# Kernel tuning notes

Measured on AMD Instinct MI355X. Metric: run time of the kernel, lower is better.

Reference implementation:

```python
import jax, jax.numpy as jnp
import numpy as np

N, E, D, H, B = 10000, 160000, 128, 1, 4
SLOPE = 0.01  # negative_slope from DeepQNet default


def gat_layer(x, node_state, src, dst, W, att_src, att_dst, Wns, bns, bias):
    # x: [N,D] or [B,N,D]; node_state: [B,N,1]
    xs = x + node_state @ Wns + bns              # [B,N,D]
    Bx, Nn = xs.shape[0], xs.shape[1]
    h = (xs @ W).reshape(Bx, Nn, H, D)           # [B,N,H,C]
    a_src = (h * att_src).sum(-1)                # [B,N,H]
    a_dst = (h * att_dst).sum(-1)                # [B,N,H]
    ae = a_src[:, src] + a_dst[:, dst]           # [B,Etot,H]
    ae = jnp.where(ae > 0, ae, SLOPE * ae)       # leaky_relu
    ae_t = jnp.moveaxis(ae, 1, 0)                # [Etot,B,H]
    m = jax.ops.segment_max(ae_t, dst, num_segments=Nn)   # [N,B,H]
    e = jnp.exp(ae_t - m[dst])
    s = jax.ops.segment_sum(e, dst, num_segments=Nn)
    alpha = e / s[dst]                           # [Etot,B,H]
    h_e = jnp.moveaxis(h, 1, 0)                  # [N,B,H,C]
    msg = alpha[..., None] * h_e[src]            # [Etot,B,H,C]
    out = jax.ops.segment_sum(msg, dst, num_segments=Nn)  # [N,B,H,C]
    out = jnp.moveaxis(out, 0, 1).mean(2) + bias # concat=False -> head mean
    return jax.nn.relu(out)


def setup_inputs() -> dict:
    key = jax.random.key(0)
    ks = jax.random.split(key, 16)
    edges = jax.random.randint(ks[0], (2, E), 0, N)
    loop = jnp.arange(N)
    edge_index = jnp.concatenate([edges, jnp.stack([loop, loop])], axis=1)  # add_self_loops
    state = jax.random.uniform(ks[1], (B, N), dtype=jnp.float32)
    strucEmb = jax.random.normal(ks[2], (N, D), dtype=jnp.float32) * 0.1
    s = 0.05
    return {
        "state": state,
        "strucEmb": strucEmb,
        "edge_index": edge_index,
        "gat_W": jax.random.normal(ks[3], (3, D, H * D), dtype=jnp.float32) * s,
        "gat_att_src": jax.random.normal(ks[4], (3, H, D), dtype=jnp.float32) * s,
        "gat_att_dst": jax.random.normal(ks[5], (3, H, D), dtype=jnp.float32) * s,
        "gat_Wns": jax.random.normal(ks[6], (3, 1, D), dtype=jnp.float32) * s,
        "gat_bns": jnp.zeros((3, D), jnp.float32),
        "gat_bias": jnp.zeros((3, D), jnp.float32),
        "W1": jax.random.normal(ks[7], (D, D), dtype=jnp.float32) * s,
        "b1": jnp.zeros((D,), jnp.float32),
        "W2": jax.random.normal(ks[8], (D, D), dtype=jnp.float32) * s,
        "b2": jnp.zeros((D,), jnp.float32),
        "W3": jax.random.normal(ks[9], (2 * D, 1), dtype=jnp.float32) * s,
        "b3": jnp.zeros((1,), jnp.float32),
    }


def reference(state, strucEmb, edge_index, gat_W, gat_att_src, gat_att_dst,
              gat_Wns, gat_bns, gat_bias, W1, b1, W2, b2, W3, b3):
    src, dst = edge_index[0], edge_index[1]
    rs = state.reshape(state.shape[0], N, 1)     # [B,N,1]
    x = strucEmb
    for l in range(3):
        x = gat_layer(x, rs, src, dst, gat_W[l], gat_att_src[l], gat_att_dst[l],
                      gat_Wns[l], gat_bns[l], gat_bias[l])
    state_emb = x.sum(1)                         # [B,D]
    beta_state = state_emb @ W1 + b1             # [B,D]
    beta_action = x @ W2 + b2                    # [B,N,D]  (is_for_learn=True path)
    expand_state = jnp.broadcast_to(beta_state[:, None, :], beta_action.shape)
    out = jax.nn.relu(jnp.concatenate([expand_state, beta_action], axis=2))
    return out @ W3 + b3                         # [B,N,1]
```

## Files before the change

kernel.cpp:

```cpp
#include <hip/hip_runtime.h>
#include <math.h>

#define N_NODES 10000
#define B_SZ 4
#define SLOPE 0.01f
#define BN (B_SZ * N_NODES)
#define PADK 136

typedef __attribute__((ext_vector_type(8))) short short8;
typedef __attribute__((ext_vector_type(4))) float float4v;

__device__ __forceinline__ unsigned short f2bf(float f) {
    unsigned u = __builtin_bit_cast(unsigned, f);
    u += 0x7fffu + ((u >> 16) & 1u);
    return (unsigned short)(u >> 16);
}
__device__ __forceinline__ float bf2f(unsigned short s) {
    unsigned u = ((unsigned)s) << 16;
    return __builtin_bit_cast(float, u);
}
__device__ __forceinline__ float bflo(unsigned u) { return __builtin_bit_cast(float, u << 16); }
__device__ __forceinline__ float bfhi(unsigned u) { return __builtin_bit_cast(float, u & 0xffff0000u); }



__global__ __launch_bounds__(256) void setup_kernel(
    const float* __restrict__ strucEmb, const float* __restrict__ state,
    const float* __restrict__ Wns0, const float* __restrict__ bns0,
    const float* __restrict__ gatW, const float* __restrict__ W2,
    unsigned short* __restrict__ XS,
    unsigned short* __restrict__ whi, unsigned short* __restrict__ wlo,
    int* deg, int* cursor, float* state_emb)
{
    int bx = blockIdx.x, tid = threadIdx.x;
    if (bx < 2500) {
        int base = (bx * 256 + tid) * 8;
        int g = base >> 7, d0 = base & 127;
        int n = g - (g / N_NODES) * N_NODES;
        float st = state[g];
        const float* se = strucEmb + (size_t)n * 128 + d0;
        const float* wp = Wns0 + d0;
        const float* bp = bns0 + d0;
        short8 v;
#pragma unroll
        for (int j = 0; j < 8; j++)
            v[j] = (short)f2bf(se[j] + st * wp[j] + bp[j]);
        *(short8*)(XS + base) = v;
    } else if (bx < 2756) {
        int i = (bx - 2500) * 256 + tid;
        int w = i >> 14, rem = i & 16383;
        int k = rem >> 7, c = rem & 127;
        const float* src = (w < 3) ? (gatW + (size_t)w * 16384) : W2;
        float v = src[k * 128 + c];
        unsigned short h = f2bf(v);
        whi[w * 16384 + c * 128 + k] = h;
        wlo[w * 16384 + c * 128 + k] = f2bf(v - bf2f(h));
    } else {
        int i = (bx - 2756) * 256 + tid;
        if (i < N_NODES) { deg[i] = 0; cursor[i] = 0; }
        if (i < 512) state_emb[i] = 0.f;
    }
}


__global__ __launch_bounds__(256) void hist_kernel(const int* __restrict__ dst, int Etot, int* deg) {
    int e = blockIdx.x * 256 + threadIdx.x;
    if (e < Etot) atomicAdd(&deg[dst[e]], 1);
}

__global__ __launch_bounds__(1024) void scan_kernel(const int* __restrict__ deg, int* __restrict__ rowOff) {
    __shared__ int wsum[16];
    int tid = threadIdx.x;
    int lane = tid & 63, wid = tid >> 6;
    int base = tid * 10;
    int v[10]; int tot = 0;
#pragma unroll
    for (int j = 0; j < 10; j++) {
        int idx = base + j;
        int d = (idx < N_NODES) ? deg[idx] : 0;
        tot += d; v[j] = tot;
    }
    int incl = tot;
    for (int off = 1; off < 64; off <<= 1) {
        int t = __shfl_up(incl, off, 64);
        if (lane >= off) incl += t;
    }
    if (lane == 63) wsum[wid] = incl;
    __syncthreads();
    if (wid == 0) {
        int wv = (lane < 16) ? wsum[lane] : 0;
        for (int off = 1; off < 16; off <<= 1) {
            int t = __shfl_up(wv, off, 64);
            if (lane >= off) wv += t;
        }
        if (lane < 16) wsum[lane] = wv;
    }
    __syncthreads();
    int waveoff = (wid > 0) ? wsum[wid - 1] : 0;
    int excl = waveoff + incl - tot;
    if (tid == 0) rowOff[0] = 0;
#pragma unroll
    for (int j = 0; j < 10; j++) {
        int idx = base + j;
        if (idx < N_NODES) rowOff[idx + 1] = excl + v[j];
    }
}

__global__ __launch_bounds__(256) void scatter_kernel(const int* __restrict__ src, const int* __restrict__ dst,
                                                      int Etot, const int* __restrict__ rowOff,
                                                      int* cursor, int* __restrict__ srcLst) {
    int e = blockIdx.x * 256 + threadIdx.x;
    if (e < Etot) {
        int d = dst[e];
        int pos = rowOff[d] + atomicAdd(&cursor[d], 1);
        srcLst[pos] = src[e];
    }
}


__global__ __launch_bounds__(256) void gemm_att_mfma(
    const unsigned short* __restrict__ XS,
    const unsigned short* __restrict__ WThi, const unsigned short* __restrict__ WTlo,
    const float* __restrict__ attS, const float* __restrict__ attD,
    unsigned short* __restrict__ Hout, float* __restrict__ aSrcP, float* __restrict__ aDstP)
{
    __shared__ __align__(16) unsigned short sCus[64 * PADK];
    __shared__ float sAs[128], sAd[128];
    __shared__ float sPart[64 * 8];

    int tid = threadIdx.x;
    int g0 = blockIdx.x * 64;
    int w = tid >> 6, lane = tid & 63;
    int quad = lane >> 4, mcol = lane & 15;

    if (tid < 128) { sAs[tid] = attS[tid]; sAd[tid] = attD[tid]; }

    float4v acc[4][2];
#pragma unroll
    for (int mt = 0; mt < 4; mt++)
#pragma unroll
        for (int nt = 0; nt < 2; nt++) acc[mt][nt] = (float4v){0.f, 0.f, 0.f, 0.f};

#pragma unroll 1
    for (int term = 0; term < 2; term++) {
        const unsigned short* WT = term ? WTlo : WThi;
        short8 Bf[4][2];
#pragma unroll
        for (int kc = 0; kc < 4; kc++)
#pragma unroll
            for (int nt = 0; nt < 2; nt++)
                Bf[kc][nt] = *(const short8*)(WT + (w * 32 + nt * 16 + mcol) * 128 + kc * 32 + quad * 8);
#pragma unroll
        for (int kc = 0; kc < 4; kc++) {
            short8 Aa[4];
#pragma unroll
            for (int mt = 0; mt < 4; mt++)
                Aa[mt] = *(const short8*)(XS + (size_t)(g0 + mt * 16 + mcol) * 128 + kc * 32 + quad * 8);
#pragma unroll
            for (int mt = 0; mt < 4; mt++)
#pragma unroll
                for (int nt = 0; nt < 2; nt++)
                    acc[mt][nt] = __builtin_amdgcn_mfma_f32_16x16x32_bf16(Aa[mt], Bf[kc][nt], acc[mt][nt], 0, 0, 0);
        }
    }

    __syncthreads();

    float pp[16], pd[16];
#pragma unroll
    for (int r16 = 0; r16 < 16; r16++) { pp[r16] = 0.f; pd[r16] = 0.f; }
#pragma unroll
    for (int mt = 0; mt < 4; mt++)
#pragma unroll
        for (int nt = 0; nt < 2; nt++)
#pragma unroll
            for (int reg = 0; reg < 4; reg++) {
                int row = mt * 16 + quad * 4 + reg;
                int col = w * 32 + nt * 16 + mcol;
                float v = acc[mt][nt][reg];
                sCus[row * PADK + col] = f2bf(v);
                pp[mt * 4 + reg] += v * sAs[col];
                pd[mt * 4 + reg] += v * sAd[col];
            }
#pragma unroll
    for (int off = 1; off < 16; off <<= 1)
#pragma unroll
        for (int r16 = 0; r16 < 16; r16++) {
            pp[r16] += __shfl_xor(pp[r16], off);
            pd[r16] += __shfl_xor(pd[r16], off);
        }
    if (mcol == 0) {
#pragma unroll
        for (int r16 = 0; r16 < 16; r16++) {
            int row = (r16 >> 2) * 16 + quad * 4 + (r16 & 3);
            sPart[row * 8 + w * 2 + 0] = pp[r16];
            sPart[row * 8 + w * 2 + 1] = pd[r16];
        }
    }
    __syncthreads();

    for (int i = tid; i < 64 * 16; i += 256) {
        int r = i >> 4, c8 = i & 15;
        uint4 u = *(uint4*)(sCus + r * PADK + c8 * 8);
        *(uint4*)(Hout + (size_t)(g0 + r) * 128 + c8 * 8) = u;
    }
    if (tid < 64) {
        float s0 = sPart[tid * 8] + sPart[tid * 8 + 2] + sPart[tid * 8 + 4] + sPart[tid * 8 + 6];
        float s1 = sPart[tid * 8 + 1] + sPart[tid * 8 + 3] + sPart[tid * 8 + 5] + sPart[tid * 8 + 7];
        aSrcP[g0 + tid] = s0;
        aDstP[g0 + tid] = s1;
    }
}


__global__ __launch_bounds__(256) void sm_agg_kernel(
    const int* __restrict__ rowOff, const int* __restrict__ srcLst,
    const float* __restrict__ aSrcP, const float* __restrict__ aDstP,
    const unsigned short* __restrict__ H,
    const float* __restrict__ bias,
    const float* __restrict__ state, const float* __restrict__ wnsN,
    const float* __restrict__ bnsN, int addNext,
    unsigned short* __restrict__ Xout)
{
    __shared__ int   sSrcB[4 * 64];
    __shared__ float sAeB[4 * 64];
    int tid = threadIdx.x;
    int w = tid >> 6, t = tid & 63;
    int blk = blockIdx.x;
    int xcd = blk & 7;
    int b = xcd >> 1;
    int n = (((xcd & 1) * (N_NODES / 8) + (blk >> 3)) << 2) + w;
    int gb = b * N_NODES;
    int start = rowOff[n], end = rowOff[n + 1];
    int cnt = end - start;
    float adst = aDstP[gb + n];
    int*   sSrc = sSrcB + w * 64;
    float* sAe  = sAeB + w * 64;
    const uint4* H4 = (const uint4*)H;

    if (cnt <= 64) {
        float ae = -1e30f;
        if (t < cnt) {
            int sn = srcLst[start + t];
            sSrc[t] = sn;
            float v = aSrcP[gb + sn] + adst;
            ae = v > 0.f ? v : SLOPE * v;
        }
        float m = ae;
        m = fmaxf(m, __shfl_xor(m, 1));  m = fmaxf(m, __shfl_xor(m, 2));
        m = fmaxf(m, __shfl_xor(m, 4));  m = fmaxf(m, __shfl_xor(m, 8));
        m = fmaxf(m, __shfl_xor(m, 16)); m = fmaxf(m, __shfl_xor(m, 32));
        float e = (t < cnt) ? __expf(ae - m) : 0.f;
        float s = e;
        s += __shfl_xor(s, 1);  s += __shfl_xor(s, 2);  s += __shfl_xor(s, 4);
        s += __shfl_xor(s, 8);  s += __shfl_xor(s, 16); s += __shfl_xor(s, 32);
        float inv = 1.f / s;
        if (t < cnt) sAe[t] = e * inv;
        int cntE = (cnt + 3) & ~3;
        if (t >= cnt && t < cntE) { sSrc[t] = n; sAe[t] = 0.f; }

        int esub = t >> 4, c16 = t & 15;
        float a0 = 0.f, a1 = 0.f, a2 = 0.f, a3 = 0.f, a4 = 0.f, a5 = 0.f, a6 = 0.f, a7 = 0.f;
        int j = 0;
        for (; j + 16 <= cntE; j += 16) {
            uint4 h[4]; float al[4];
#pragma unroll
            for (int r = 0; r < 4; r++) {
                int jj = j + r * 4 + esub;
                h[r] = H4[(size_t)(gb + sSrc[jj]) * 16 + c16];
                al[r] = sAe[jj];
            }
#pragma unroll
            for (int r = 0; r < 4; r++) {
                a0 += al[r] * bflo(h[r].x); a1 += al[r] * bfhi(h[r].x);
                a2 += al[r] * bflo(h[r].y); a3 += al[r] * bfhi(h[r].y);
                a4 += al[r] * bflo(h[r].z); a5 += al[r] * bfhi(h[r].z);
                a6 += al[r] * bflo(h[r].w); a7 += al[r] * bfhi(h[r].w);
            }
        }
        for (; j < cntE; j += 4) {
            int jj = j + esub;
            uint4 hv = H4[(size_t)(gb + sSrc[jj]) * 16 + c16];
            float al = sAe[jj];
            a0 += al * bflo(hv.x); a1 += al * bfhi(hv.x);
            a2 += al * bflo(hv.y); a3 += al * bfhi(hv.y);
            a4 += al * bflo(hv.z); a5 += al * bfhi(hv.z);
            a6 += al * bflo(hv.w); a7 += al * bfhi(hv.w);
        }
        a0 += __shfl_xor(a0, 16); a1 += __shfl_xor(a1, 16);
        a2 += __shfl_xor(a2, 16); a3 += __shfl_xor(a3, 16);
        a4 += __shfl_xor(a4, 16); a5 += __shfl_xor(a5, 16);
        a6 += __shfl_xor(a6, 16); a7 += __shfl_xor(a7, 16);
        a0 += __shfl_xor(a0, 32); a1 += __shfl_xor(a1, 32);
        a2 += __shfl_xor(a2, 32); a3 += __shfl_xor(a3, 32);
        a4 += __shfl_xor(a4, 32); a5 += __shfl_xor(a5, 32);
        a6 += __shfl_xor(a6, 32); a7 += __shfl_xor(a7, 32);
        if (esub == 0) {
            int d0 = c16 * 8;
            float o0 = fmaxf(a0 + bias[d0],     0.f);
            float o1 = fmaxf(a1 + bias[d0 + 1], 0.f);
            float o2 = fmaxf(a2 + bias[d0 + 2], 0.f);
            float o3 = fmaxf(a3 + bias[d0 + 3], 0.f);
            float o4 = fmaxf(a4 + bias[d0 + 4], 0.f);
            float o5 = fmaxf(a5 + bias[d0 + 5], 0.f);
            float o6 = fmaxf(a6 + bias[d0 + 6], 0.f);
            float o7 = fmaxf(a7 + bias[d0 + 7], 0.f);
            if (addNext) {
                float st = state[gb + n];
                o0 += st * wnsN[d0]     + bnsN[d0];
                o1 += st * wnsN[d0 + 1] + bnsN[d0 + 1];
                o2 += st * wnsN[d0 + 2] + bnsN[d0 + 2];
                o3 += st * wnsN[d0 + 3] + bnsN[d0 + 3];
                o4 += st * wnsN[d0 + 4] + bnsN[d0 + 4];
                o5 += st * wnsN[d0 + 5] + bnsN[d0 + 5];
                o6 += st * wnsN[d0 + 6] + bnsN[d0 + 6];
                o7 += st * wnsN[d0 + 7] + bnsN[d0 + 7];
            }
            uint4 u;
            u.x = (unsigned)f2bf(o0) | ((unsigned)f2bf(o1) << 16);
            u.y = (unsigned)f2bf(o2) | ((unsigned)f2bf(o3) << 16);
            u.z = (unsigned)f2bf(o4) | ((unsigned)f2bf(o5) << 16);
            u.w = (unsigned)f2bf(o6) | ((unsigned)f2bf(o7) << 16);
            ((uint4*)Xout)[(size_t)(gb + n) * 16 + c16] = u;
        }
    } else {
        const unsigned* Hu = (const unsigned*)H;
        float m = -1e30f;
        for (int i = start + t; i < end; i += 64) {
            int sn = srcLst[i];
            float v = aSrcP[gb + sn] + adst;
            m = fmaxf(m, v > 0.f ? v : SLOPE * v);
        }
        m = fmaxf(m, __shfl_xor(m, 1));  m = fmaxf(m, __shfl_xor(m, 2));
        m = fmaxf(m, __shfl_xor(m, 4));  m = fmaxf(m, __shfl_xor(m, 8));
        m = fmaxf(m, __shfl_xor(m, 16)); m = fmaxf(m, __shfl_xor(m, 32));
        float s = 0.f;
        for (int i = start + t; i < end; i += 64) {
            int sn = srcLst[i];
            float v = aSrcP[gb + sn] + adst;
            float ae2 = v > 0.f ? v : SLOPE * v;
            s += __expf(ae2 - m);
        }
        s += __shfl_xor(s, 1);  s += __shfl_xor(s, 2);  s += __shfl_xor(s, 4);
        s += __shfl_xor(s, 8);  s += __shfl_xor(s, 16); s += __shfl_xor(s, 32);
        float inv = 1.f / s;
        float accx = 0.f, accy = 0.f;
        for (int c0 = start; c0 < end; c0 += 64) {
            int c = min(64, end - c0);
            if (t < c) {
                int sn = srcLst[c0 + t];
                sSrc[t] = sn;
                float v = aSrcP[gb + sn] + adst;
                float ae2 = v > 0.f ? v : SLOPE * v;
                sAe[t] = __expf(ae2 - m);
            }
            for (int j = 0; j < c; j++) {
                float a0 = sAe[j];
                unsigned h0 = Hu[(size_t)(gb + sSrc[j]) * 64 + t];
                accx += a0 * bflo(h0);
                accy += a0 * bfhi(h0);
            }
        }
        float ox = fmaxf(accx * inv + bias[2 * t], 0.f);
        float oy = fmaxf(accy * inv + bias[2 * t + 1], 0.f);
        if (addNext) {
            float st = state[gb + n];
            ox += st * wnsN[2 * t]     + bnsN[2 * t];
            oy += st * wnsN[2 * t + 1] + bnsN[2 * t + 1];
        }
        ((unsigned*)Xout)[(size_t)(gb + n) * 64 + t] =
            (unsigned)f2bf(ox) | ((unsigned)f2bf(oy) << 16);
    }
}


__global__ __launch_bounds__(128) void sum_nodes_kernel(const unsigned short* __restrict__ X, float* state_emb) {
    int cx = blockIdx.x, b = blockIdx.y, d = threadIdx.x;
    int n0 = cx * 157, n1 = n0 + 157;
    if (n1 > N_NODES) n1 = N_NODES;
    float acc = 0.f;
    for (int n = n0; n < n1; n++) acc += bf2f(X[(size_t)(b * N_NODES + n) * 128 + d]);
    atomicAdd(&state_emb[b * 128 + d], acc);
}


__global__ __launch_bounds__(256) void final_mfma(
    const unsigned short* __restrict__ X,
    const unsigned short* __restrict__ WThi, const unsigned short* __restrict__ WTlo,
    const float* __restrict__ b2, const float* __restrict__ W3,
    const float* __restrict__ b3,
    const float* __restrict__ state_emb, const float* __restrict__ W1,
    const float* __restrict__ b1,
    float* __restrict__ out)
{
    __shared__ float sB2[128], sW3[128];
    __shared__ float sPart[64 * 4];
    __shared__ float sC1p[8], sC1[4];

    int tid = threadIdx.x;
    int g0 = blockIdx.x * 64;
    int w = tid >> 6, lane = tid & 63;
    int quad = lane >> 4, mcol = lane & 15;

    if (tid < 128) { sB2[tid] = b2[tid]; sW3[tid] = W3[128 + tid]; }

    {
        int d = tid & 127;
        int bh = tid >> 7;
        float p0 = b1[d], p1 = b1[d];
        for (int k = 0; k < 128; k++) {
            float wv = W1[k * 128 + d];
            p0 += state_emb[bh * 128 + k] * wv;
            p1 += state_emb[(bh + 2) * 128 + k] * wv;
        }
        float w3d = W3[d];
        p0 = fmaxf(p0, 0.f) * w3d;
        p1 = fmaxf(p1, 0.f) * w3d;
#pragma unroll
        for (int off = 1; off < 64; off <<= 1) {
            p0 += __shfl_xor(p0, off);
            p1 += __shfl_xor(p1, off);
        }
        if (lane == 0) { sC1p[w * 2 + 0] = p0; sC1p[w * 2 + 1] = p1; }
    }
    __syncthreads();
    if (tid == 0) {
        sC1[0] = sC1p[0] + sC1p[2];  sC1[2] = sC1p[1] + sC1p[3];
        sC1[1] = sC1p[4] + sC1p[6];  sC1[3] = sC1p[5] + sC1p[7];
    }

    float4v acc[4][2];
#pragma unroll
    for (int mt = 0; mt < 4; mt++)
#pragma unroll
        for (int nt = 0; nt < 2; nt++) acc[mt][nt] = (float4v){0.f, 0.f, 0.f, 0.f};

#pragma unroll 1
    for (int term = 0; term < 2; term++) {
        const unsigned short* WT = term ? WTlo : WThi;
        short8 Bf[4][2];
#pragma unroll
        for (int kc = 0; kc < 4; kc++)
#pragma unroll
            for (int nt = 0; nt < 2; nt++)
                Bf[kc][nt] = *(const short8*)(WT + (w * 32 + nt * 16 + mcol) * 128 + kc * 32 + quad * 8);
#pragma unroll
        for (int kc = 0; kc < 4; kc++) {
            short8 Aa[4];
#pragma unroll
            for (int mt = 0; mt < 4; mt++)
                Aa[mt] = *(const short8*)(X + (size_t)(g0 + mt * 16 + mcol) * 128 + kc * 32 + quad * 8);
#pragma unroll
            for (int mt = 0; mt < 4; mt++)
#pragma unroll
                for (int nt = 0; nt < 2; nt++)
                    acc[mt][nt] = __builtin_amdgcn_mfma_f32_16x16x32_bf16(Aa[mt], Bf[kc][nt], acc[mt][nt], 0, 0, 0);
        }
    }

    float pp[16];
#pragma unroll
    for (int r16 = 0; r16 < 16; r16++) pp[r16] = 0.f;
#pragma unroll
    for (int mt = 0; mt < 4; mt++)
#pragma unroll
        for (int nt = 0; nt < 2; nt++)
#pragma unroll
            for (int reg = 0; reg < 4; reg++) {
                int col = w * 32 + nt * 16 + mcol;
                float v = acc[mt][nt][reg] + sB2[col];
                v = v > 0.f ? v : 0.f;
                pp[mt * 4 + reg] += v * sW3[col];
            }
#pragma unroll
    for (int off = 1; off < 16; off <<= 1)
#pragma unroll
        for (int r16 = 0; r16 < 16; r16++)
            pp[r16] += __shfl_xor(pp[r16], off);
    if (mcol == 0) {
#pragma unroll
        for (int r16 = 0; r16 < 16; r16++) {
            int row = (r16 >> 2) * 16 + quad * 4 + (r16 & 3);
            sPart[row * 4 + w] = pp[r16];
        }
    }
    __syncthreads();
    if (tid < 64) {
        float p = sPart[tid * 4] + sPart[tid * 4 + 1] + sPart[tid * 4 + 2] + sPart[tid * 4 + 3];
        int g = g0 + tid;
        int b = g / N_NODES;
        out[g] = p + sC1[b] + b3[0];
    }
}


extern "C" void kernel_launch(void* const* d_in, const int* in_sizes, int n_in,
                              void* d_out, int out_size, void* d_ws, size_t ws_size,
                              hipStream_t stream) {
    const float* state    = (const float*)d_in[0];
    const float* strucEmb = (const float*)d_in[1];
    const int*   edge_idx = (const int*)d_in[2];
    const float* gat_W    = (const float*)d_in[3];
    const float* gat_aS   = (const float*)d_in[4];
    const float* gat_aD   = (const float*)d_in[5];
    const float* gat_Wns  = (const float*)d_in[6];
    const float* gat_bns  = (const float*)d_in[7];
    const float* gat_bias = (const float*)d_in[8];
    const float* W1 = (const float*)d_in[9];
    const float* b1 = (const float*)d_in[10];
    const float* W2 = (const float*)d_in[11];
    const float* b2 = (const float*)d_in[12];
    const float* W3 = (const float*)d_in[13];
    const float* b3 = (const float*)d_in[14];
    float* out = (float*)d_out;

    int Etot = in_sizes[2] / 2;
    const int* srcArr = edge_idx;
    const int* dstArr = edge_idx + Etot;

    float* ws = (float*)d_ws;
    unsigned short* Xb = (unsigned short*)ws;
    unsigned short* Hb = (unsigned short*)(ws + 2560000);
    float* aSrcP       = ws + 5120000;
    float* aDstP       = ws + 5160000;
    float* state_emb   = ws + 5200000;
    unsigned short* whi = (unsigned short*)(ws + 5200516);
    unsigned short* wlo = whi + 4 * 16384;
    int*   iws         = (int*)(ws + 5200516 + 65536);
    int*   rowOff      = iws;
    int*   deg         = iws + 10001;
    int*   cursor      = deg + 10000;
    int*   srcLst      = cursor + 10000;

    setup_kernel<<<2796, 256, 0, stream>>>(strucEmb, state, gat_Wns, gat_bns,
                                           gat_W, W2, Xb, whi, wlo, deg, cursor, state_emb);
    hist_kernel<<<(Etot + 255) / 256, 256, 0, stream>>>(dstArr, Etot, deg);
    scan_kernel<<<1, 1024, 0, stream>>>(deg, rowOff);
    scatter_kernel<<<(Etot + 255) / 256, 256, 0, stream>>>(srcArr, dstArr, Etot, rowOff, cursor, srcLst);

    for (int l = 0; l < 3; l++) {
        gemm_att_mfma<<<BN / 64, 256, 0, stream>>>(
            Xb, whi + (size_t)l * 16384, wlo + (size_t)l * 16384,
            gat_aS + l * 128, gat_aD + l * 128, Hb, aSrcP, aDstP);
        sm_agg_kernel<<<N_NODES, 256, 0, stream>>>(
            rowOff, srcLst, aSrcP, aDstP, Hb, gat_bias + l * 128,
            state, gat_Wns + (l + 1 < 3 ? (l + 1) * 128 : 0),
            gat_bns + (l + 1 < 3 ? (l + 1) * 128 : 0), (l < 2) ? 1 : 0, Xb);
    }

    sum_nodes_kernel<<<dim3(64, B_SZ), 128, 0, stream>>>(Xb, state_emb);
    final_mfma<<<BN / 64, 256, 0, stream>>>(Xb, whi + 3 * 16384, wlo + 3 * 16384,
                                            b2, W3, b3, state_emb, W1, b1, out);
}
```

Baseline: 323.4 us.

## Fuse per-layer GEMM, aggregation and final head into one persistent kernel

Replaces the eight per-layer and final kernel launches with one persistent kernel of 512 blocks. The blocks loop over GEMM tiles and aggregation items and separate phases with a software grid barrier built on global atomics. This removes launch overhead and the gaps between kernels. In exchange it relies on all 512 blocks being co-resident, which risks deadlock if they are not, and it limits parallelism per phase to the fixed grid.

```diff
diff --git a/kernel.cpp b/kernel.cpp
--- a/kernel.cpp
+++ b/kernel.cpp
@@ -6,6 +6,7 @@
 #define SLOPE 0.01f
 #define BN (B_SZ * N_NODES)
 #define PADK 136
+#define GRID_P 512
 
 typedef __attribute__((ext_vector_type(8))) short short8;
 typedef __attribute__((ext_vector_type(4))) float float4v;
@@ -21,6 +22,24 @@
 }
 __device__ __forceinline__ float bflo(unsigned u) { return __builtin_bit_cast(float, u << 16); }
 __device__ __forceinline__ float bfhi(unsigned u) { return __builtin_bit_cast(float, u & 0xffff0000u); }
+
+__device__ __forceinline__ void grid_barrier(int* counter, int* gen) {
+    __syncthreads();
+    if (threadIdx.x == 0) {
+        __threadfence();
+        int g0 = __hip_atomic_load(gen, __ATOMIC_RELAXED, __HIP_MEMORY_SCOPE_AGENT);
+        int arrived = __hip_atomic_fetch_add(counter, 1, __ATOMIC_ACQ_REL, __HIP_MEMORY_SCOPE_AGENT);
+        if (arrived == GRID_P - 1) {
+            __hip_atomic_store(counter, 0, __ATOMIC_RELAXED, __HIP_MEMORY_SCOPE_AGENT);
+            __hip_atomic_store(gen, g0 + 1, __ATOMIC_RELEASE, __HIP_MEMORY_SCOPE_AGENT);
+        } else {
+            while (__hip_atomic_load(gen, __ATOMIC_ACQUIRE, __HIP_MEMORY_SCOPE_AGENT) == g0)
+                __builtin_amdgcn_s_sleep(2);
+        }
+        __threadfence();
+    }
+    __syncthreads();
+}
 
 
 
@@ -30,7 +49,7 @@
     const float* __restrict__ gatW, const float* __restrict__ W2,
     unsigned short* __restrict__ XS,
     unsigned short* __restrict__ whi, unsigned short* __restrict__ wlo,
-    int* deg, int* cursor, float* state_emb)
+    int* deg, int* cursor, float* state_emb, int* barrier_ws)
 {
     int bx = blockIdx.x, tid = threadIdx.x;
     if (bx < 2500) {
@@ -59,6 +78,7 @@
         int i = (bx - 2756) * 256 + tid;
         if (i < N_NODES) { deg[i] = 0; cursor[i] = 0; }
         if (i < 512) state_emb[i] = 0.f;
+        if (i < 2) barrier_ws[i] = 0;
     }
 }
 
@@ -118,378 +138,401 @@
 }
 
 
-__global__ __launch_bounds__(256) void gemm_att_mfma(
-    const unsigned short* __restrict__ XS,
-    const unsigned short* __restrict__ WThi, const unsigned short* __restrict__ WTlo,
-    const float* __restrict__ attS, const float* __restrict__ attD,
-    unsigned short* __restrict__ Hout, float* __restrict__ aSrcP, float* __restrict__ aDstP)
+__global__ __launch_bounds__(256, 2) void mega_kernel(
+    const unsigned short* __restrict__ whi_all, const unsigned short* __restrict__ wlo_all,
+    unsigned short* __restrict__ Xb, unsigned short* __restrict__ Hb,
+    float* __restrict__ aSrcP, float* __restrict__ aDstP,
+    const int* __restrict__ rowOff, const int* __restrict__ srcLst,
+    const float* __restrict__ gat_aS, const float* __restrict__ gat_aD,
+    const float* __restrict__ gat_bias,
+    const float* __restrict__ state, const float* __restrict__ gat_Wns,
+    const float* __restrict__ gat_bns,
+    float* __restrict__ state_emb,
+    const float* __restrict__ b2a, const float* __restrict__ W3,
+    const float* __restrict__ b3,
+    const float* __restrict__ W1, const float* __restrict__ b1,
+    float* __restrict__ out, int* barrier_ws)
 {
-    __shared__ __align__(16) unsigned short sCus[64 * PADK];
-    __shared__ float sAs[128], sAd[128];
-    __shared__ float sPart[64 * 8];
+    __shared__ __align__(16) unsigned char smem[20480];
+    int* bar_cnt = barrier_ws;
+    int* bar_gen = barrier_ws + 1;
 
     int tid = threadIdx.x;
-    int g0 = blockIdx.x * 64;
     int w = tid >> 6, lane = tid & 63;
     int quad = lane >> 4, mcol = lane & 15;
-
-    if (tid < 128) { sAs[tid] = attS[tid]; sAd[tid] = attD[tid]; }
-
-    float4v acc[4][2];
-#pragma unroll
-    for (int mt = 0; mt < 4; mt++)
-#pragma unroll
-        for (int nt = 0; nt < 2; nt++) acc[mt][nt] = (float4v){0.f, 0.f, 0.f, 0.f};
+    int bid = blockIdx.x;
+
+    for (int l = 0; l < 3; l++) {
+        {
+            unsigned short* sCus = (unsigned short*)smem;
+            float* sAs   = (float*)(smem + 17408);
+            float* sAd   = (float*)(smem + 17920);
+            float* sPart = (float*)(smem + 18432);
+
+            if (tid < 128) { sAs[tid] = gat_aS[l * 128 + tid]; sAd[tid] = gat_aD[l * 128 + tid]; }
+            __syncthreads();
+
+            const unsigned short* WThi = whi_all + (size_t)l * 16384;
+            const unsigned short* WTlo = wlo_all + (size_t)l * 16384;
+
+            for (int tile = bid; tile < BN / 64; tile += GRID_P) {
+                int g0 = tile * 64;
+
+                float4v acc[4][2];
+#pragma unroll
+                for (int mt = 0; mt < 4; mt++)
+#pragma unroll
+                    for (int nt = 0; nt < 2; nt++) acc[mt][nt] = (float4v){0.f, 0.f, 0.f, 0.f};
 
 #pragma unroll 1
-    for (int term = 0; term < 2; term++) {
-        const unsigned short* WT = term ? WTlo : WThi;
-        short8 Bf[4][2];
-#pragma unroll
-        for (int kc = 0; kc < 4; kc++)
-#pragma unroll
-            for (int nt = 0; nt < 2; nt++)
-                Bf[kc][nt] = *(const short8*)(WT + (w * 32 + nt * 16 + mcol) * 128 + kc * 32 + quad * 8);
-#pragma unroll
-        for (int kc = 0; kc < 4; kc++) {
-            short8 Aa[4];
+                for (int term = 0; term < 2; term++) {
+                    const unsigned short* WT = term ? WTlo : WThi;
+                    short8 Bf[4][2];
+#pragma unroll
+                    for (int kc = 0; kc < 4; kc++)
+#pragma unroll
+                        for (int nt = 0; nt < 2; nt++)
+                            Bf[kc][nt] = *(const short8*)(WT + (w * 32 + nt * 16 + mcol) * 128 + kc * 32 + quad * 8);
+#pragma unroll
+                    for (int kc = 0; kc < 4; kc++) {
+                        short8 Aa[4];
+#pragma unroll
+                        for (int mt = 0; mt < 4; mt++)
+                            Aa[mt] = *(const short8*)(Xb + (size_t)(g0 + mt * 16 + mcol) * 128 + kc * 32 + quad * 8);
+#pragma unroll
+                        for (int mt = 0; mt < 4; mt++)
+#pragma unroll
+                            for (int nt = 0; nt < 2; nt++)
+                                acc[mt][nt] = __builtin_amdgcn_mfma_f32_16x16x32_bf16(Aa[mt], Bf[kc][nt], acc[mt][nt], 0, 0, 0);
+                    }
+                }
+
+                float pp[16], pd[16];
+#pragma unroll
+                for (int r16 = 0; r16 < 16; r16++) { pp[r16] = 0.f; pd[r16] = 0.f; }
+#pragma unroll
+                for (int mt = 0; mt < 4; mt++)
+#pragma unroll
+                    for (int nt = 0; nt < 2; nt++)
+#pragma unroll
+                        for (int reg = 0; reg < 4; reg++) {
+                            int row = mt * 16 + quad * 4 + reg;
+                            int col = w * 32 + nt * 16 + mcol;
+                            float v = acc[mt][nt][reg];
+                            sCus[row * PADK + col] = f2bf(v);
+                            pp[mt * 4 + reg] += v * sAs[col];
+                            pd[mt * 4 + reg] += v * sAd[col];
+                        }
+#pragma unroll
+                for (int off = 1; off < 16; off <<= 1)
+#pragma unroll
+                    for (int r16 = 0; r16 < 16; r16++) {
+                        pp[r16] += __shfl_xor(pp[r16], off);
+                        pd[r16] += __shfl_xor(pd[r16], off);
+                    }
+                if (mcol == 0) {
+#pragma unroll
+                    for (int r16 = 0; r16 < 16; r16++) {
+                        int row = (r16 >> 2) * 16 + quad * 4 + (r16 & 3);
+                        sPart[row * 8 + w * 2 + 0] = pp[r16];
+                        sPart[row * 8 + w * 2 + 1] = pd[r16];
+                    }
+                }
+                __syncthreads();
+
+                for (int i = tid; i < 64 * 16; i += 256) {
+                    int r = i >> 4, c8 = i & 15;
+                    uint4 u = *(uint4*)(sCus + r * PADK + c8 * 8);
+                    *(uint4*)(Hb + (size_t)(g0 + r) * 128 + c8 * 8) = u;
+                }
+                if (tid < 64) {
+                    float s0 = sPart[tid * 8] + sPart[tid * 8 + 2] + sPart[tid * 8 + 4] + sPart[tid * 8 + 6];
+                    float s1 = sPart[tid * 8 + 1] + sPart[tid * 8 + 3] + sPart[tid * 8 + 5] + sPart[tid * 8 + 7];
+                    aSrcP[g0 + tid] = s0;
+                    aDstP[g0 + tid] = s1;
+                }
+                __syncthreads();
+            }
+        }
+        grid_barrier(bar_cnt, bar_gen);
+
+        {
+            int*   sSrc = (int*)smem + w * 64;
+            float* sAe  = (float*)(smem + 1024) + w * 64;
+            const float* bias = gat_bias + l * 128;
+            const float* wnsN = gat_Wns + (l + 1 < 3 ? (l + 1) * 128 : 0);
+            const float* bnsN = gat_bns + (l + 1 < 3 ? (l + 1) * 128 : 0);
+            int addNext = (l < 2) ? 1 : 0;
+            const uint4* H4 = (const uint4*)Hb;
+
+            int gwv = bid * 4 + w;
+            for (int item = gwv; item < BN; item += GRID_P * 4) {
+                int b = item / N_NODES;
+                int n = item - b * N_NODES;
+                int gb = b * N_NODES;
+                int t = lane;
+                int start = rowOff[n], end = rowOff[n + 1];
+                int cnt = end - start;
+                float adst = aDstP[gb + n];
+
+                if (cnt <= 64) {
+                    float ae = -1e30f;
+                    if (t < cnt) {
+                        int sn = srcLst[start + t];
+                        sSrc[t] = sn;
+                        float v = aSrcP[gb + sn] + adst;
+                        ae = v > 0.f ? v : SLOPE * v;
+                    }
+                    float m = ae;
+                    m = fmaxf(m, __shfl_xor(m, 1));  m = fmaxf(m, __shfl_xor(m, 2));
+                    m = fmaxf(m, __shfl_xor(m, 4));  m = fmaxf(m, __shfl_xor(m, 8));
+                    m = fmaxf(m, __shfl_xor(m, 16)); m = fmaxf(m, __shfl_xor(m, 32));
+                    float e = (t < cnt) ? __expf(ae - m) : 0.f;
+                    float s = e;
+                    s += __shfl_xor(s, 1);  s += __shfl_xor(s, 2);  s += __shfl_xor(s, 4);
+                    s += __shfl_xor(s, 8);  s += __shfl_xor(s, 16); s += __shfl_xor(s, 32);
+                    float inv = 1.f / s;
+                    if (t < cnt) sAe[t] = e * inv;
+                    int cntE = (cnt + 3) & ~3;
+                    if (t >= cnt && t < cntE) { sSrc[t] = n; sAe[t] = 0.f; }
+
+                    int esub = t >> 4, c16 = t & 15;
+                    float a0 = 0.f, a1 = 0.f, a2 = 0.f, a3 = 0.f, a4 = 0.f, a5 = 0.f, a6 = 0.f, a7 = 0.f;
+                    int j = 0;
+                    for (; j + 16 <= cntE; j += 16) {
+                        uint4 h[4]; float al[4];
+#pragma unroll
+                        for (int r = 0; r < 4; r++) {
+                            int jj = j + r * 4 + esub;
+                            h[r] = H4[(size_t)(gb + sSrc[jj]) * 16 + c16];
+                            al[r] = sAe[jj];
+                        }
+#pragma unroll
+                        for (int r = 0; r < 4; r++) {
+                            a0 += al[r] * bflo(h[r].x); a1 += al[r] * bfhi(h[r].x);
+                            a2 += al[r] * bflo(h[r].y); a3 += al[r] * bfhi(h[r].y);
+                            a4 += al[r] * bflo(h[r].z); a5 += al[r] * bfhi(h[r].z);
+                            a6 += al[r] * bflo(h[r].w); a7 += al[r] * bfhi(h[r].w);
+                        }
+                    }
+                    for (; j < cntE; j += 4) {
+                        int jj = j + esub;
+                        uint4 hv = H4[(size_t)(gb + sSrc[jj]) * 16 + c16];
+                        float al = sAe[jj];
+                        a0 += al * bflo(hv.x); a1 += al * bfhi(hv.x);
+                        a2 += al * bflo(hv.y); a3 += al * bfhi(hv.y);
+                        a4 += al * bflo(hv.z); a5 += al * bfhi(hv.z);
+                        a6 += al * bflo(hv.w); a7 += al * bfhi(hv.w);
+                    }
+                    a0 += __shfl_xor(a0, 16); a1 += __shfl_xor(a1, 16);
+                    a2 += __shfl_xor(a2, 16); a3 += __shfl_xor(a3, 16);
+                    a4 += __shfl_xor(a4, 16); a5 += __shfl_xor(a5, 16);
+                    a6 += __shfl_xor(a6, 16); a7 += __shfl_xor(a7, 16);
+                    a0 += __shfl_xor(a0, 32); a1 += __shfl_xor(a1, 32);
+                    a2 += __shfl_xor(a2, 32); a3 += __shfl_xor(a3, 32);
+                    a4 += __shfl_xor(a4, 32); a5 += __shfl_xor(a5, 32);
+                    a6 += __shfl_xor(a6, 32); a7 += __shfl_xor(a7, 32);
+                    if (esub == 0) {
+                        int d0 = c16 * 8;
+                        float o0 = fmaxf(a0 + bias[d0],     0.f);
+                        float o1 = fmaxf(a1 + bias[d0 + 1], 0.f);
+                        float o2 = fmaxf(a2 + bias[d0 + 2], 0.f);
+                        float o3 = fmaxf(a3 + bias[d0 + 3], 0.f);
+                        float o4 = fmaxf(a4 + bias[d0 + 4], 0.f);
+                        float o5 = fmaxf(a5 + bias[d0 + 5], 0.f);
+                        float o6 = fmaxf(a6 + bias[d0 + 6], 0.f);
+                        float o7 = fmaxf(a7 + bias[d0 + 7], 0.f);
+                        if (addNext) {
+                            float st = state[gb + n];
+                            o0 += st * wnsN[d0]     + bnsN[d0];
+                            o1 += st * wnsN[d0 + 1] + bnsN[d0 + 1];
+                            o2 += st * wnsN[d0 + 2] + bnsN[d0 + 2];
+                            o3 += st * wnsN[d0 + 3] + bnsN[d0 + 3];
+                            o4 += st * wnsN[d0 + 4] + bnsN[d0 + 4];
+                            o5 += st * wnsN[d0 + 5] + bnsN[d0 + 5];
+                            o6 += st * wnsN[d0 + 6] + bnsN[d0 + 6];
+                            o7 += st * wnsN[d0 + 7] + bnsN[d0 + 7];
+                        }
+                        uint4 u;
+                        u.x = (unsigned)f2bf(o0) | ((unsigned)f2bf(o1) << 16);
+                        u.y = (unsigned)f2bf(o2) | ((unsigned)f2bf(o3) << 16);
+                        u.z = (unsigned)f2bf(o4) | ((unsigned)f2bf(o5) << 16);
+                        u.w = (unsigned)f2bf(o6) | ((unsigned)f2bf(o7) << 16);
+                        ((uint4*)Xb)[(size_t)(gb + n) * 16 + c16] = u;
+                    }
+                } else {
+                    const unsigned* Hu = (const unsigned*)Hb;
+                    int t2 = lane;
+                    float m = -1e30f;
+                    for (int i = start + t2; i < end; i += 64) {
+                        int sn = srcLst[i];
+                        float v = aSrcP[gb + sn] + adst;
+                        m = fmaxf(m, v > 0.f ? v : SLOPE * v);
+                    }
+                    m = fmaxf(m, __shfl_xor(m, 1));  m = fmaxf(m, __shfl_xor(m, 2));
+                    m = fmaxf(m, __shfl_xor(m, 4));  m = fmaxf(m, __shfl_xor(m, 8));
+                    m = fmaxf(m, __shfl_xor(m, 16)); m = fmaxf(m, __shfl_xor(m, 32));
+                    float s = 0.f;
+                    for (int i = start + t2; i < end; i += 64) {
+                        int sn = srcLst[i];
+                        float v = aSrcP[gb + sn] + adst;
+                        float ae2 = v > 0.f ? v : SLOPE * v;
+                        s += __expf(ae2 - m);
+                    }
+                    s += __shfl_xor(s, 1);  s += __shfl_xor(s, 2);  s += __shfl_xor(s, 4);
+                    s += __shfl_xor(s, 8);  s += __shfl_xor(s, 16); s += __shfl_xor(s, 32);
+                    float inv = 1.f / s;
+                    float accx = 0.f, accy = 0.f;
+                    for (int c0 = start; c0 < end; c0 += 64) {
+                        int c = min(64, end - c0);
+                        if (t2 < c) {
+                            int sn = srcLst[c0 + t2];
+                            sSrc[t2] = sn;
+                            float v = aSrcP[gb + sn] + adst;
+                            float ae2 = v > 0.f ? v : SLOPE * v;
+                            sAe[t2] = __expf(ae2 - m);
+                        }
+                        for (int j = 0; j < c; j++) {
+                            float a0 = sAe[j];
+                            unsigned h0 = Hu[(size_t)(gb + sSrc[j]) * 64 + t2];
+                            accx += a0 * bflo(h0);
+                            accy += a0 * bfhi(h0);
+                        }
+                    }
+                    float ox = fmaxf(accx * inv + bias[2 * t2], 0.f);
+                    float oy = fmaxf(accy * inv + bias[2 * t2 + 1], 0.f);
+                    if (addNext) {
+                        float st = state[gb + n];
+                        ox += st * wnsN[2 * t2]     + bnsN[2 * t2];
+                        oy += st * wnsN[2 * t2 + 1] + bnsN[2 * t2 + 1];
+                    }
+                    ((unsigned*)Xb)[(size_t)(gb + n) * 64 + t2] =
+                        (unsigned)f2bf(ox) | ((unsigned)f2bf(oy) << 16);
+                }
+            }
+        }
+        grid_barrier(bar_cnt, bar_gen);
+    }
+
+    {
+        int item = bid;
+        int b = item >> 7, cx = item & 127;
+        int n0 = cx * 79;
+        int n1 = n0 + 79; if (n1 > N_NODES) n1 = N_NODES;
+        if (tid < 128 && n0 < N_NODES) {
+            float acc = 0.f;
+            for (int n = n0; n < n1; n++)
+                acc += bf2f(Xb[(size_t)(b * N_NODES + n) * 128 + tid]);
+            atomicAdd(&state_emb[b * 128 + tid], acc);
+        }
+    }
+    grid_barrier(bar_cnt, bar_gen);
+
+    {
+        float* sB2  = (float*)smem;
+        float* sW3  = (float*)(smem + 512);
+        float* sPf  = (float*)(smem + 1024);
+        float* sC1p = (float*)(smem + 2048);
+        float* sC1  = (float*)(smem + 2080);
+
+        if (tid < 128) { sB2[tid] = b2a[tid]; sW3[tid] = W3[128 + tid]; }
+
+        {
+            int d = tid & 127;
+            int bh = tid >> 7;
+            float p0 = b1[d], p1 = b1[d];
+            for (int k = 0; k < 128; k++) {
+                float wv = W1[k * 128 + d];
+                p0 += state_emb[bh * 128 + k] * wv;
+                p1 += state_emb[(bh + 2) * 128 + k] * wv;
+            }
+            float w3d = W3[d];
+            p0 = fmaxf(p0, 0.f) * w3d;
+            p1 = fmaxf(p1, 0.f) * w3d;
+#pragma unroll
+            for (int off = 1; off < 64; off <<= 1) {
+                p0 += __shfl_xor(p0, off);
+                p1 += __shfl_xor(p1, off);
+            }
+            if (lane == 0) { sC1p[w * 2 + 0] = p0; sC1p[w * 2 + 1] = p1; }
+        }
+        __syncthreads();
+        if (tid == 0) {
+            sC1[0] = sC1p[0] + sC1p[2];  sC1[2] = sC1p[1] + sC1p[3];
+            sC1[1] = sC1p[4] + sC1p[6];  sC1[3] = sC1p[5] + sC1p[7];
+        }
+        __syncthreads();
+
+        const unsigned short* WThi = whi_all + (size_t)3 * 16384;
+        const unsigned short* WTlo = wlo_all + (size_t)3 * 16384;
+
+        for (int tile = bid; tile < BN / 64; tile += GRID_P) {
+            int g0 = tile * 64;
+
+            float4v acc[4][2];
 #pragma unroll
             for (int mt = 0; mt < 4; mt++)
-                Aa[mt] = *(const short8*)(XS + (size_t)(g0 + mt * 16 + mcol) * 128 + kc * 32 + quad * 8);
+#pragma unroll
+                for (int nt = 0; nt < 2; nt++) acc[mt][nt] = (float4v){0.f, 0.f, 0.f, 0.f};
+
+#pragma unroll 1
+            for (int term = 0; term < 2; term++) {
+                const unsigned short* WT = term ? WTlo : WThi;
+                short8 Bf[4][2];
+#pragma unroll
+                for (int kc = 0; kc < 4; kc++)
+#pragma unroll
+                    for (int nt = 0; nt < 2; nt++)
+                        Bf[kc][nt] = *(const short8*)(WT + (w * 32 + nt * 16 + mcol) * 128 + kc * 32 + quad * 8);
+#pragma unroll
+                for (int kc = 0; kc < 4; kc++) {
+                    short8 Aa[4];
+#pragma unroll
+                    for (int mt = 0; mt < 4; mt++)
+                        Aa[mt] = *(const short8*)(Xb + (size_t)(g0 + mt * 16 + mcol) * 128 + kc * 32 + quad * 8);
+#pragma unroll
+                    for (int mt = 0; mt < 4; mt++)
+#pragma unroll
+                        for (int nt = 0; nt < 2; nt++)
+                            acc[mt][nt] = __builtin_amdgcn_mfma_f32_16x16x32_bf16(Aa[mt], Bf[kc][nt], acc[mt][nt], 0, 0, 0);
+                }
+            }
+
+            float pp[16];
+#pragma unroll
+            for (int r16 = 0; r16 < 16; r16++) pp[r16] = 0.f;
 #pragma unroll
             for (int mt = 0; mt < 4; mt++)
 #pragma unroll
                 for (int nt = 0; nt < 2; nt++)
-                    acc[mt][nt] = __builtin_amdgcn_mfma_f32_16x16x32_bf16(Aa[mt], Bf[kc][nt], acc[mt][nt], 0, 0, 0);
-        }
-    }
-
-    __syncthreads();
-
-    float pp[16], pd[16];
-#pragma unroll
-    for (int r16 = 0; r16 < 16; r16++) { pp[r16] = 0.f; pd[r16] = 0.f; }
-#pragma unroll
-    for (int mt = 0; mt < 4; mt++)
-#pragma unroll
-        for (int nt = 0; nt < 2; nt++)
-#pragma unroll
-            for (int reg = 0; reg < 4; reg++) {
-                int row = mt * 16 + quad * 4 + reg;
-                int col = w * 32 + nt * 16 + mcol;
-                float v = acc[mt][nt][reg];
-                sCus[row * PADK + col] = f2bf(v);
-                pp[mt * 4 + reg] += v * sAs[col];
-                pd[mt * 4 + reg] += v * sAd[col];
-            }
-#pragma unroll
-    for (int off = 1; off < 16; off <<= 1)
-#pragma unroll
-        for (int r16 = 0; r16 < 16; r16++) {
-            pp[r16] += __shfl_xor(pp[r16], off);
-            pd[r16] += __shfl_xor(pd[r16], off);
-        }
-    if (mcol == 0) {
-#pragma unroll
-        for (int r16 = 0; r16 < 16; r16++) {
-            int row = (r16 >> 2) * 16 + quad * 4 + (r16 & 3);
-            sPart[row * 8 + w * 2 + 0] = pp[r16];
-            sPart[row * 8 + w * 2 + 1] = pd[r16];
-        }
-    }
-    __syncthreads();
-
-    for (int i = tid; i < 64 * 16; i += 256) {
-        int r = i >> 4, c8 = i & 15;
-        uint4 u = *(uint4*)(sCus + r * PADK + c8 * 8);
-        *(uint4*)(Hout + (size_t)(g0 + r) * 128 + c8 * 8) = u;
-    }
-    if (tid < 64) {
-        float s0 = sPart[tid * 8] + sPart[tid * 8 + 2] + sPart[tid * 8 + 4] + sPart[tid * 8 + 6];
-        float s1 = sPart[tid * 8 + 1] + sPart[tid * 8 + 3] + sPart[tid * 8 + 5] + sPart[tid * 8 + 7];
-        aSrcP[g0 + tid] = s0;
-        aDstP[g0 + tid] = s1;
-    }
-}
-
-
-__global__ __launch_bounds__(256) void sm_agg_kernel(
-    const int* __restrict__ rowOff, const int* __restrict__ srcLst,
-    const float* __restrict__ aSrcP, const float* __restrict__ aDstP,
-    const unsigned short* __restrict__ H,
-    const float* __restrict__ bias,
-    const float* __restrict__ state, const float* __restrict__ wnsN,
-    const float* __restrict__ bnsN, int addNext,
-    unsigned short* __restrict__ Xout)
-{
-    __shared__ int   sSrcB[4 * 64];
-    __shared__ float sAeB[4 * 64];
-    int tid = threadIdx.x;
-    int w = tid >> 6, t = tid & 63;
-    int blk = blockIdx.x;
-    int xcd = blk & 7;
-    int b = xcd >> 1;
-    int n = (((xcd & 1) * (N_NODES / 8) + (blk >> 3)) << 2) + w;
-    int gb = b * N_NODES;
-    int start = rowOff[n], end = rowOff[n + 1];
-    int cnt = end - start;
-    float adst = aDstP[gb + n];
-    int*   sSrc = sSrcB + w * 64;
-    float* sAe  = sAeB + w * 64;
-    const uint4* H4 = (const uint4*)H;
-
-    if (cnt <= 64) {
-        float ae = -1e30f;
-        if (t < cnt) {
-            int sn = srcLst[start + t];
-            sSrc[t] = sn;
-            float v = aSrcP[gb + sn] + adst;
-            ae = v > 0.f ? v : SLOPE * v;
-        }
-        float m = ae;
-        m = fmaxf(m, __shfl_xor(m, 1));  m = fmaxf(m, __shfl_xor(m, 2));
-        m = fmaxf(m, __shfl_xor(m, 4));  m = fmaxf(m, __shfl_xor(m, 8));
-        m = fmaxf(m, __shfl_xor(m, 16)); m = fmaxf(m, __shfl_xor(m, 32));
-        float e = (t < cnt) ? __expf(ae - m) : 0.f;
-        float s = e;
-        s += __shfl_xor(s, 1);  s += __shfl_xor(s, 2);  s += __shfl_xor(s, 4);
-        s += __shfl_xor(s, 8);  s += __shfl_xor(s, 16); s += __shfl_xor(s, 32);
-        float inv = 1.f / s;
-        if (t < cnt) sAe[t] = e * inv;
-        int cntE = (cnt + 3) & ~3;
-        if (t >= cnt && t < cntE) { sSrc[t] = n; sAe[t] = 0.f; }
-
-        int esub = t >> 4, c16 = t & 15;
-        float a0 = 0.f, a1 = 0.f, a2 = 0.f, a3 = 0.f, a4 = 0.f, a5 = 0.f, a6 = 0.f, a7 = 0.f;
-        int j = 0;
-        for (; j + 16 <= cntE; j += 16) {
-            uint4 h[4]; float al[4];
-#pragma unroll
-            for (int r = 0; r < 4; r++) {
-                int jj = j + r * 4 + esub;
-                h[r] = H4[(size_t)(gb + sSrc[jj]) * 16 + c16];
-                al[r] = sAe[jj];
-            }
-#pragma unroll
-            for (int r = 0; r < 4; r++) {
-                a0 += al[r] * bflo(h[r].x); a1 += al[r] * bfhi(h[r].x);
-                a2 += al[r] * bflo(h[r].y); a3 += al[r] * bfhi(h[r].y);
-                a4 += al[r] * bflo(h[r].z); a5 += al[r] * bfhi(h[r].z);
-                a6 += al[r] * bflo(h[r].w); a7 += al[r] * bfhi(h[r].w);
-            }
-        }
-        for (; j < cntE; j += 4) {
-            int jj = j + esub;
-            uint4 hv = H4[(size_t)(gb + sSrc[jj]) * 16 + c16];
-            float al = sAe[jj];
-            a0 += al * bflo(hv.x); a1 += al * bfhi(hv.x);
-            a2 += al * bflo(hv.y); a3 += al * bfhi(hv.y);
-            a4 += al * bflo(hv.z); a5 += al * bfhi(hv.z);
-            a6 += al * bflo(hv.w); a7 += al * bfhi(hv.w);
-        }
-        a0 += __shfl_xor(a0, 16); a1 += __shfl_xor(a1, 16);
-        a2 += __shfl_xor(a2, 16); a3 += __shfl_xor(a3, 16);
-        a4 += __shfl_xor(a4, 16); a5 += __shfl_xor(a5, 16);
-        a6 += __shfl_xor(a6, 16); a7 += __shfl_xor(a7, 16);
-        a0 += __shfl_xor(a0, 32); a1 += __shfl_xor(a1, 32);
-        a2 += __shfl_xor(a2, 32); a3 += __shfl_xor(a3, 32);
-        a4 += __shfl_xor(a4, 32); a5 += __shfl_xor(a5, 32);
-        a6 += __shfl_xor(a6, 32); a7 += __shfl_xor(a7, 32);
-        if (esub == 0) {
-            int d0 = c16 * 8;
-            float o0 = fmaxf(a0 + bias[d0],     0.f);
-            float o1 = fmaxf(a1 + bias[d0 + 1], 0.f);
-            float o2 = fmaxf(a2 + bias[d0 + 2], 0.f);
-            float o3 = fmaxf(a3 + bias[d0 + 3], 0.f);
-            float o4 = fmaxf(a4 + bias[d0 + 4], 0.f);
-            float o5 = fmaxf(a5 + bias[d0 + 5], 0.f);
-            float o6 = fmaxf(a6 + bias[d0 + 6], 0.f);
-            float o7 = fmaxf(a7 + bias[d0 + 7], 0.f);
-            if (addNext) {
-                float st = state[gb + n];
-                o0 += st * wnsN[d0]     + bnsN[d0];
-                o1 += st * wnsN[d0 + 1] + bnsN[d0 + 1];
-                o2 += st * wnsN[d0 + 2] + bnsN[d0 + 2];
-                o3 += st * wnsN[d0 + 3] + bnsN[d0 + 3];
-                o4 += st * wnsN[d0 + 4] + bnsN[d0 + 4];
-                o5 += st * wnsN[d0 + 5] + bnsN[d0 + 5];
-                o6 += st * wnsN[d0 + 6] + bnsN[d0 + 6];
-                o7 += st * wnsN[d0 + 7] + bnsN[d0 + 7];
-            }
-            uint4 u;
-            u.x = (unsigned)f2bf(o0) | ((unsigned)f2bf(o1) << 16);
-            u.y = (unsigned)f2bf(o2) | ((unsigned)f2bf(o3) << 16);
-            u.z = (unsigned)f2bf(o4) | ((unsigned)f2bf(o5) << 16);
-            u.w = (unsigned)f2bf(o6) | ((unsigned)f2bf(o7) << 16);
-            ((uint4*)Xout)[(size_t)(gb + n) * 16 + c16] = u;
-        }
-    } else {
-        const unsigned* Hu = (const unsigned*)H;
-        float m = -1e30f;
-        for (int i = start + t; i < end; i += 64) {
-            int sn = srcLst[i];
-            float v = aSrcP[gb + sn] + adst;
-            m = fmaxf(m, v > 0.f ? v : SLOPE * v);
-        }
-        m = fmaxf(m, __shfl_xor(m, 1));  m = fmaxf(m, __shfl_xor(m, 2));
-        m = fmaxf(m, __shfl_xor(m, 4));  m = fmaxf(m, __shfl_xor(m, 8));
-        m = fmaxf(m, __shfl_xor(m, 16)); m = fmaxf(m, __shfl_xor(m, 32));
-        float s = 0.f;
-        for (int i = start + t; i < end; i += 64) {
-            int sn = srcLst[i];
-            float v = aSrcP[gb + sn] + adst;
-            float ae2 = v > 0.f ? v : SLOPE * v;
-            s += __expf(ae2 - m);
-        }
-        s += __shfl_xor(s, 1);  s += __shfl_xor(s, 2);  s += __shfl_xor(s, 4);
-        s += __shfl_xor(s, 8);  s += __shfl_xor(s, 16); s += __shfl_xor(s, 32);
-        float inv = 1.f / s;
-        float accx = 0.f, accy = 0.f;
-        for (int c0 = start; c0 < end; c0 += 64) {
-            int c = min(64, end - c0);
-            if (t < c) {
-                int sn = srcLst[c0 + t];
-                sSrc[t] = sn;
-                float v = aSrcP[gb + sn] + adst;
-                float ae2 = v > 0.f ? v : SLOPE * v;
-                sAe[t] = __expf(ae2 - m);
-            }
-            for (int j = 0; j < c; j++) {
-                float a0 = sAe[j];
-                unsigned h0 = Hu[(size_t)(gb + sSrc[j]) * 64 + t];
-                accx += a0 * bflo(h0);
-                accy += a0 * bfhi(h0);
-            }
-        }
-        float ox = fmaxf(accx * inv + bias[2 * t], 0.f);
-        float oy = fmaxf(accy * inv + bias[2 * t + 1], 0.f);
-        if (addNext) {
-            float st = state[gb + n];
-            ox += st * wnsN[2 * t]     + bnsN[2 * t];
-            oy += st * wnsN[2 * t + 1] + bnsN[2 * t + 1];
-        }
-        ((unsigned*)Xout)[(size_t)(gb + n) * 64 + t] =
-            (unsigned)f2bf(ox) | ((unsigned)f2bf(oy) << 16);
-    }
-}
-
-
-__global__ __launch_bounds__(128) void sum_nodes_kernel(const unsigned short* __restrict__ X, float* state_emb) {
-    int cx = blockIdx.x, b = blockIdx.y, d = threadIdx.x;
-    int n0 = cx * 157, n1 = n0 + 157;
-    if (n1 > N_NODES) n1 = N_NODES;
-    float acc = 0.f;
-    for (int n = n0; n < n1; n++) acc += bf2f(X[(size_t)(b * N_NODES + n) * 128 + d]);
-    atomicAdd(&state_emb[b * 128 + d], acc);
-}
-
-
-__global__ __launch_bounds__(256) void final_mfma(
-    const unsigned short* __restrict__ X,
-    const unsigned short* __restrict__ WThi, const unsigned short* __restrict__ WTlo,
-    const float* __restrict__ b2, const float* __restrict__ W3,
-    const float* __restrict__ b3,
-    const float* __restrict__ state_emb, const float* __restrict__ W1,
-    const float* __restrict__ b1,
-    float* __restrict__ out)
-{
-    __shared__ float sB2[128], sW3[128];
-    __shared__ float sPart[64 * 4];
-    __shared__ float sC1p[8], sC1[4];
-
-    int tid = threadIdx.x;
-    int g0 = blockIdx.x * 64;
-    int w = tid >> 6, lane = tid & 63;
-    int quad = lane >> 4, mcol = lane & 15;
-
-    if (tid < 128) { sB2[tid] = b2[tid]; sW3[tid] = W3[128 + tid]; }
-
-    {
-        int d = tid & 127;
-        int bh = tid >> 7;
-        float p0 = b1[d], p1 = b1[d];
-        for (int k = 0; k < 128; k++) {
-            float wv = W1[k * 128 + d];
-            p0 += state_emb[bh * 128 + k] * wv;
-            p1 += state_emb[(bh + 2) * 128 + k] * wv;
-        }
-        float w3d = W3[d];
-        p0 = fmaxf(p0, 0.f) * w3d;
-        p1 = fmaxf(p1, 0.f) * w3d;
-#pragma unroll
-        for (int off = 1; off < 64; off <<= 1) {
-            p0 += __shfl_xor(p0, off);
-            p1 += __shfl_xor(p1, off);
-        }
-        if (lane == 0) { sC1p[w * 2 + 0] = p0; sC1p[w * 2 + 1] = p1; }
-    }
-    __syncthreads();
-    if (tid == 0) {
-        sC1[0] = sC1p[0] + sC1p[2];  sC1[2] = sC1p[1] + sC1p[3];
-        sC1[1] = sC1p[4] + sC1p[6];  sC1[3] = sC1p[5] + sC1p[7];
-    }
-
-    float4v acc[4][2];
-#pragma unroll
-    for (int mt = 0; mt < 4; mt++)
-#pragma unroll
-        for (int nt = 0; nt < 2; nt++) acc[mt][nt] = (float4v){0.f, 0.f, 0.f, 0.f};
-
-#pragma unroll 1
-    for (int term = 0; term < 2; term++) {
-        const unsigned short* WT = term ? WTlo : WThi;
-        short8 Bf[4][2];
-#pragma unroll
-        for (int kc = 0; kc < 4; kc++)
-#pragma unroll
-            for (int nt = 0; nt < 2; nt++)
-                Bf[kc][nt] = *(const short8*)(WT + (w * 32 + nt * 16 + mcol) * 128 + kc * 32 + quad * 8);
-#pragma unroll
-        for (int kc = 0; kc < 4; kc++) {
-            short8 Aa[4];
-#pragma unroll
-            for (int mt = 0; mt < 4; mt++)
-                Aa[mt] = *(const short8*)(X + (size_t)(g0 + mt * 16 + mcol) * 128 + kc * 32 + quad * 8);
-#pragma unroll
-            for (int mt = 0; mt < 4; mt++)
-#pragma unroll
-                for (int nt = 0; nt < 2; nt++)
-                    acc[mt][nt] = __builtin_amdgcn_mfma_f32_16x16x32_bf16(Aa[mt], Bf[kc][nt], acc[mt][nt], 0, 0, 0);
-        }
-    }
-
-    float pp[16];
-#pragma unroll
-    for (int r16 = 0; r16 < 16; r16++) pp[r16] = 0.f;
-#pragma unroll
-    for (int mt = 0; mt < 4; mt++)
-#pragma unroll
-        for (int nt = 0; nt < 2; nt++)
-#pragma unroll
-            for (int reg = 0; reg < 4; reg++) {
-                int col = w * 32 + nt * 16 + mcol;
-                float v = acc[mt][nt][reg] + sB2[col];
-                v = v > 0.f ? v : 0.f;
-                pp[mt * 4 + reg] += v * sW3[col];
-            }
-#pragma unroll
-    for (int off = 1; off < 16; off <<= 1)
-#pragma unroll
-        for (int r16 = 0; r16 < 16; r16++)
-            pp[r16] += __shfl_xor(pp[r16], off);
-    if (mcol == 0) {
-#pragma unroll
-        for (int r16 = 0; r16 < 16; r16++) {
-            int row = (r16 >> 2) * 16 + quad * 4 + (r16 & 3);
-            sPart[row * 4 + w] = pp[r16];
-        }
-    }
-    __syncthreads();
-    if (tid < 64) {
-        float p = sPart[tid * 4] + sPart[tid * 4 + 1] + sPart[tid * 4 + 2] + sPart[tid * 4 + 3];
-        int g = g0 + tid;
-        int b = g / N_NODES;
-        out[g] = p + sC1[b] + b3[0];
+#pragma unroll
+                    for (int reg = 0; reg < 4; reg++) {
+                        int col = w * 32 + nt * 16 + mcol;
+                        float v = acc[mt][nt][reg] + sB2[col];
+                        v = v > 0.f ? v : 0.f;
+                        pp[mt * 4 + reg] += v * sW3[col];
+                    }
+#pragma unroll
+            for (int off = 1; off < 16; off <<= 1)
+#pragma unroll
+                for (int r16 = 0; r16 < 16; r16++)
+                    pp[r16] += __shfl_xor(pp[r16], off);
+            if (mcol == 0) {
+#pragma unroll
+                for (int r16 = 0; r16 < 16; r16++) {
+                    int row = (r16 >> 2) * 16 + quad * 4 + (r16 & 3);
+                    sPf[row * 4 + w] = pp[r16];
+                }
+            }
+            __syncthreads();
+            if (tid < 64) {
+                float p = sPf[tid * 4] + sPf[tid * 4 + 1] + sPf[tid * 4 + 2] + sPf[tid * 4 + 3];
+                int g = g0 + tid;
+                int b = g / N_NODES;
+                out[g] = p + sC1[b] + b3[0];
+            }
+            __syncthreads();
+        }
     }
 }
 
@@ -530,25 +573,17 @@
     int*   rowOff      = iws;
     int*   deg         = iws + 10001;
     int*   cursor      = deg + 10000;
-    int*   srcLst      = cursor + 10000;
+    int*   barrier_ws  = cursor + 10000;
+    int*   srcLst      = barrier_ws + 2;
 
     setup_kernel<<<2796, 256, 0, stream>>>(strucEmb, state, gat_Wns, gat_bns,
-                                           gat_W, W2, Xb, whi, wlo, deg, cursor, state_emb);
+                                           gat_W, W2, Xb, whi, wlo, deg, cursor, state_emb, barrier_ws);
     hist_kernel<<<(Etot + 255) / 256, 256, 0, stream>>>(dstArr, Etot, deg);
     scan_kernel<<<1, 1024, 0, stream>>>(deg, rowOff);
     scatter_kernel<<<(Etot + 255) / 256, 256, 0, stream>>>(srcArr, dstArr, Etot, rowOff, cursor, srcLst);
 
-    for (int l = 0; l < 3; l++) {
-        gemm_att_mfma<<<BN / 64, 256, 0, stream>>>(
-            Xb, whi + (size_t)l * 16384, wlo + (size_t)l * 16384,
-            gat_aS + l * 128, gat_aD + l * 128, Hb, aSrcP, aDstP);
-        sm_agg_kernel<<<N_NODES, 256, 0, stream>>>(
-            rowOff, srcLst, aSrcP, aDstP, Hb, gat_bias + l * 128,
-            state, gat_Wns + (l + 1 < 3 ? (l + 1) * 128 : 0),
-            gat_bns + (l + 1 < 3 ? (l + 1) * 128 : 0), (l < 2) ? 1 : 0, Xb);
-    }
-
-    sum_nodes_kernel<<<dim3(64, B_SZ), 128, 0, stream>>>(Xb, state_emb);
-    final_mfma<<<BN / 64, 256, 0, stream>>>(Xb, whi + 3 * 16384, wlo + 3 * 16384,
-                                            b2, W3, b3, state_emb, W1, b1, out);
-}
+    mega_kernel<<<GRID_P, 256, 0, stream>>>(
+        whi, wlo, Xb, Hb, aSrcP, aDstP, rowOff, srcLst,
+        gat_aS, gat_aD, gat_bias, state, gat_Wns, gat_bns,
+        state_emb, b2, W3, b3, W1, b1, out, barrier_ws);
+}
```

Result: slower. 1.108 ms (+242.6%).
